# Optimization experiments

Measured on AMD Instinct MI355X. Metric: run time of the kernel, lower is better.

The kernel has to match this reference:

```python
import jax, jax.numpy as jnp
import numpy as np

B, S, D_DIM = 32, 512, 1024

def setup_inputs() -> dict:
    key = jax.random.key(0)
    k1, k2, k3, k4 = jax.random.split(key, 4)
    return {
        "D": jax.random.normal(k1, (B, S, D_DIM), dtype=jnp.float32),
        "H": jax.random.normal(k2, (B, S, D_DIM), dtype=jnp.float32),
        # learned params: U is (d+1, d) (xavier-style scale), W is (2d+1,)
        # (original inits W to zeros; we use small random values so the linear
        #  term is exercised — same math either way)
        "U": jax.random.normal(k3, (D_DIM + 1, D_DIM), dtype=jnp.float32) * 0.02,
        "W": jax.random.normal(k4, (2 * D_DIM + 1,), dtype=jnp.float32) * 0.02,
    }

def reference(D, H, U, W):
    # D, H: [B, S, d]; U: [d+1, d]; W: [2d+1]
    d = H.shape[-1]
    ones = jnp.ones(D.shape[:2] + (1,), dtype=D.dtype)
    Daug = jnp.concatenate([D, ones], axis=-1)              # [B, S, d+1]
    # bilinear term: v.U.u  -> [B, Sx, Sy]
    bil = jnp.einsum('bxi,ij,byj->bxy', Daug, U, H)
    # linear term W . concat(D_aug, H): algebraically split — avoids the
    # O(B*S*S*2d) concatenated intermediate of the original implementation
    lin = (Daug @ W[:d + 1])[:, :, None] + (H @ W[d + 1:])[:, None, :]
    return bil + lin
```

## Files before the change

kernel.cpp:

```cpp
#include <hip/hip_runtime.h>


#define D_DIM 1024
#define ROWS 16384

typedef float floatx4 __attribute__((ext_vector_type(4)));
typedef __bf16 bf16x8 __attribute__((ext_vector_type(8)));

__device__ inline unsigned short f2bf(float f) {
  unsigned int u = __builtin_bit_cast(unsigned int, f);
  u = (u + 0x7FFFu + ((u >> 16) & 1u)) >> 16;
  return (unsigned short)u;
}

__device__ inline void async_load16(const void* g, void* l) {
  __builtin_amdgcn_global_load_lds(
      (const __attribute__((address_space(1))) void*)g,
      (__attribute__((address_space(3))) void*)l, 16, 0, 0);
}

__global__ __launch_bounds__(256) void cast_rows_kernel(
    const float* __restrict__ D, const float* __restrict__ H,
    const float* __restrict__ W,
    unsigned short* __restrict__ Dbf, unsigned short* __restrict__ Hbf,
    float* __restrict__ linD, float* __restrict__ linH) {
  int rowid = blockIdx.x;
  bool isH = rowid >= ROWS;
  int r = isH ? rowid - ROWS : rowid;
  const float* src = (isH ? H : D) + (size_t)r * D_DIM;
  unsigned short* dst = (isH ? Hbf : Dbf) + (size_t)r * D_DIM;
  const float* w = W + (isH ? (D_DIM + 1) : 0);
  int t = threadIdx.x;
  float4 v = ((const float4*)src)[t];
  float s = v.x * w[4*t] + v.y * w[4*t+1] + v.z * w[4*t+2] + v.w * w[4*t+3];
  ushort4 o;
  o.x = f2bf(v.x); o.y = f2bf(v.y); o.z = f2bf(v.z); o.w = f2bf(v.w);
  ((ushort4*)dst)[t] = o;
  #pragma unroll
  for (int off = 32; off > 0; off >>= 1) s += __shfl_down(s, off, 64);
  __shared__ float red[4];
  int wave = t >> 6;
  if ((t & 63) == 0) red[wave] = s;
  __syncthreads();
  if (t == 0) {
    float tot = red[0] + red[1] + red[2] + red[3];
    if (!isH) tot += W[D_DIM];
    (isH ? linH : linD)[r] = tot;
  }
}

__global__ __launch_bounds__(256) void transU_kernel(
    const float* __restrict__ U, unsigned short* __restrict__ Ut) {
  __shared__ float tile[32][33];
  int n0 = blockIdx.x * 32;
  int k0 = blockIdx.y * 32;
  int t = threadIdx.x;
  int tr = t >> 5, tc = t & 31;
  #pragma unroll
  for (int i = 0; i < 32; i += 8)
    tile[tr + i][tc] = U[(size_t)(k0 + tr + i) * D_DIM + n0 + tc];
  __syncthreads();
  #pragma unroll
  for (int i = 0; i < 32; i += 8)
    Ut[(size_t)(n0 + tr + i) * D_DIM + k0 + tc] = f2bf(tile[tc][tr + i]);
}

template <int MWAVES, int NWAVES, int MT, int NT, int BROWS>
__device__ inline void gemm_core_swz(
    const unsigned short* __restrict__ A, const unsigned short* __restrict__ Bt,
    int m0, int n0, unsigned short* As, unsigned short* Bs,
    floatx4 (&acc)[MT][NT]) {
  const int K = D_DIM;
  int tid = threadIdx.x;
  int l = tid & 63, wave = tid >> 6;
  int quad = l >> 4, lrow = l & 15;
  int wm = (NWAVES == 2) ? (wave >> 1) : wave;
  int wn = (NWAVES == 2) ? (wave & 1) : 0;

  int srow = 8 * wave + (l >> 3);
  int sq = (l & 7) ^ (l >> 3);
  const unsigned short* gA = A + (size_t)(m0 + srow) * K + sq * 8;
  const unsigned short* gB = Bt + (size_t)(n0 + srow) * K + sq * 8;

  int rl = lrow & 7, gofs = lrow >> 3;
  int baseA = wm * (MT * 128) + gofs * 64 + rl * 8;
  int baseB = wn * (NT * 128) + gofs * 64 + rl * 8;

  for (int k0 = 0; k0 < K; k0 += 64) {
    __syncthreads();
    #pragma unroll
    for (int j = 0; j < 4; ++j)
      async_load16(gA + (size_t)(32 * j) * K + k0, As + (j * 256 + tid) * 8);
    #pragma unroll
    for (int j = 0; j < BROWS / 32; ++j)
      async_load16(gB + (size_t)(32 * j) * K + k0, Bs + (j * 256 + tid) * 8);
    __syncthreads();
    #pragma unroll
    for (int s = 0; s < 2; ++s) {
      int xq = (s * 4 + quad) ^ rl;
      bf16x8 a[MT], b[NT];
      #pragma unroll
      for (int mt = 0; mt < MT; ++mt)
        a[mt] = *(const bf16x8*)(As + (baseA + mt * 128 + xq) * 8);
      #pragma unroll
      for (int nt = 0; nt < NT; ++nt)
        b[nt] = *(const bf16x8*)(Bs + (baseB + nt * 128 + xq) * 8);
      #pragma unroll
      for (int mt = 0; mt < MT; ++mt)
        #pragma unroll
        for (int nt = 0; nt < NT; ++nt)
          acc[mt][nt] = __builtin_amdgcn_mfma_f32_16x16x32_bf16(
              a[mt], b[nt], acc[mt][nt], 0, 0, 0);
    }
  }
}

__global__ __launch_bounds__(256) void gemm1_kernel(
    const unsigned short* __restrict__ A,
    const unsigned short* __restrict__ Bt,
    const float* __restrict__ Ubias,
    unsigned short* __restrict__ T) {
  __shared__ __align__(16) unsigned short As[128 * 64];
  __shared__ __align__(16) unsigned short Bs[128 * 64];
  int m0 = blockIdx.x * 128, n0 = blockIdx.y * 128;
  int tid = threadIdx.x;
  int lane = tid & 63, wave = tid >> 6;
  int quad = lane >> 4, lrow = lane & 15;
  int wm = wave >> 1, wn = wave & 1;

  floatx4 acc[4][4] = {};
  gemm_core_swz<2, 2, 4, 4, 128>(A, Bt, m0, n0, As, Bs, acc);

  #pragma unroll
  for (int mt = 0; mt < 4; ++mt)
    #pragma unroll
    for (int nt = 0; nt < 4; ++nt) {
      int row = m0 + wm * 64 + mt * 16 + quad * 4;
      int col = n0 + wn * 64 + nt * 16 + lrow;
      float bias = Ubias[col];
      #pragma unroll
      for (int rr = 0; rr < 4; ++rr)
        T[(size_t)(row + rr) * D_DIM + col] = f2bf(acc[mt][nt][rr] + bias);
    }
}

__global__ __launch_bounds__(256) void gemm2_kernel(
    const unsigned short* __restrict__ Tg,
    const unsigned short* __restrict__ Hbf,
    const float* __restrict__ linD, const float* __restrict__ linH,
    float* __restrict__ out) {
  __shared__ __align__(16) unsigned short As[128 * 64];
  __shared__ __align__(16) unsigned short Bs[64 * 64];
  int b = blockIdx.x;
  int t = blockIdx.y;
  int m0 = (t >> 3) * 128, n0 = (t & 7) * 64;
  const unsigned short* A = Tg + (size_t)b * 512 * D_DIM;
  const unsigned short* Bt = Hbf + (size_t)b * 512 * D_DIM;
  int tid = threadIdx.x;
  int lane = tid & 63, wave = tid >> 6;
  int quad = lane >> 4, lrow = lane & 15;
  int wm = wave;

  floatx4 acc[2][4] = {};
  gemm_core_swz<4, 1, 2, 4, 64>(A, Bt, m0, n0, As, Bs, acc);

  #pragma unroll
  for (int mt = 0; mt < 2; ++mt)
    #pragma unroll
    for (int nt = 0; nt < 4; ++nt) {
      int row = m0 + wm * 32 + mt * 16 + quad * 4;
      int col = n0 + nt * 16 + lrow;
      float lh = linH[b * 512 + col];
      #pragma unroll
      for (int rr = 0; rr < 4; ++rr) {
        float v = acc[mt][nt][rr] + linD[b * 512 + row + rr] + lh;
        out[((size_t)b * 512 + row + rr) * 512 + col] = v;
      }
    }
}

extern "C" void kernel_launch(void* const* d_in, const int* in_sizes, int n_in,
                              void* d_out, int out_size, void* d_ws, size_t ws_size,
                              hipStream_t stream) {
  const float* D = (const float*)d_in[0];
  const float* H = (const float*)d_in[1];
  const float* U = (const float*)d_in[2];
  const float* W = (const float*)d_in[3];
  float* out = (float*)d_out;

  char* ws = (char*)d_ws;
  unsigned short* Dbf = (unsigned short*)ws; ws += (size_t)ROWS * D_DIM * 2;
  unsigned short* Hbf = (unsigned short*)ws; ws += (size_t)ROWS * D_DIM * 2;
  unsigned short* Tbf = (unsigned short*)ws; ws += (size_t)ROWS * D_DIM * 2;
  unsigned short* Ut  = (unsigned short*)ws; ws += (size_t)D_DIM * D_DIM * 2;
  float* linD = (float*)ws;                  ws += (size_t)ROWS * 4;
  float* linH = (float*)ws;                  ws += (size_t)ROWS * 4;

  cast_rows_kernel<<<dim3(2 * ROWS), 256, 0, stream>>>(D, H, W, Dbf, Hbf, linD, linH);
  transU_kernel<<<dim3(32, 32), 256, 0, stream>>>(U, Ut);
  gemm1_kernel<<<dim3(128, 8), 256, 0, stream>>>(Dbf, Ut, U + (size_t)D_DIM * D_DIM, Tbf);
  gemm2_kernel<<<dim3(32, 32), 256, 0, stream>>>(Tbf, Hbf, linD, linH, out);
}
```

Before: 234.1 us.

## Merge cast and U-transpose kernels, enlarge gemm2 tile, use nontemporal output stores

Folds the U transpose/cast into the row-cast kernel as extra blocks, which saves one launch. The batched second GEMM moves from 128x64 to 128x128 tiles with a 2x2 wave layout, which raises arithmetic intensity and cuts redundant A-tile loads. The grid halves to 512 blocks on the GPU's 256 CUs. Output stores become nontemporal so the large fp32 result does not pollute cache. The bigger accumulators raise register pressure, and the smaller grid may hurt occupancy.

```diff
diff --git a/kernel.cpp b/kernel.cpp
--- a/kernel.cpp
+++ b/kernel.cpp
@@ -19,50 +19,51 @@
       (__attribute__((address_space(3))) void*)l, 16, 0, 0);
 }
 
-__global__ __launch_bounds__(256) void cast_rows_kernel(
+__global__ __launch_bounds__(256) void cast_transU_kernel(
     const float* __restrict__ D, const float* __restrict__ H,
-    const float* __restrict__ W,
+    const float* __restrict__ U, const float* __restrict__ W,
     unsigned short* __restrict__ Dbf, unsigned short* __restrict__ Hbf,
+    unsigned short* __restrict__ Ut,
     float* __restrict__ linD, float* __restrict__ linH) {
-  int rowid = blockIdx.x;
-  bool isH = rowid >= ROWS;
-  int r = isH ? rowid - ROWS : rowid;
-  const float* src = (isH ? H : D) + (size_t)r * D_DIM;
-  unsigned short* dst = (isH ? Hbf : Dbf) + (size_t)r * D_DIM;
-  const float* w = W + (isH ? (D_DIM + 1) : 0);
+  __shared__ float tile[32][33];
+  int bid = blockIdx.x;
   int t = threadIdx.x;
-  float4 v = ((const float4*)src)[t];
-  float s = v.x * w[4*t] + v.y * w[4*t+1] + v.z * w[4*t+2] + v.w * w[4*t+3];
-  ushort4 o;
-  o.x = f2bf(v.x); o.y = f2bf(v.y); o.z = f2bf(v.z); o.w = f2bf(v.w);
-  ((ushort4*)dst)[t] = o;
-  #pragma unroll
-  for (int off = 32; off > 0; off >>= 1) s += __shfl_down(s, off, 64);
-  __shared__ float red[4];
-  int wave = t >> 6;
-  if ((t & 63) == 0) red[wave] = s;
-  __syncthreads();
-  if (t == 0) {
-    float tot = red[0] + red[1] + red[2] + red[3];
-    if (!isH) tot += W[D_DIM];
-    (isH ? linH : linD)[r] = tot;
+
+  if (bid < 2 * ROWS) {
+    bool isH = bid >= ROWS;
+    int r = isH ? bid - ROWS : bid;
+    const float* src = (isH ? H : D) + (size_t)r * D_DIM;
+    unsigned short* dst = (isH ? Hbf : Dbf) + (size_t)r * D_DIM;
+    const float* w = W + (isH ? (D_DIM + 1) : 0);
+    float4 v = ((const float4*)src)[t];
+    float s = v.x * w[4*t] + v.y * w[4*t+1] + v.z * w[4*t+2] + v.w * w[4*t+3];
+    ushort4 o;
+    o.x = f2bf(v.x); o.y = f2bf(v.y); o.z = f2bf(v.z); o.w = f2bf(v.w);
+    ((ushort4*)dst)[t] = o;
+    #pragma unroll
+    for (int off = 32; off > 0; off >>= 1) s += __shfl_down(s, off, 64);
+    float* red = &tile[0][0];
+    int wave = t >> 6;
+    if ((t & 63) == 0) red[wave] = s;
+    __syncthreads();
+    if (t == 0) {
+      float tot = red[0] + red[1] + red[2] + red[3];
+      if (!isH) tot += W[D_DIM];
+      (isH ? linH : linD)[r] = tot;
+    }
+  } else {
+    int tb = bid - 2 * ROWS;
+    int n0 = (tb & 31) * 32;
+    int k0 = (tb >> 5) * 32;
+    int tr = t >> 5, tc = t & 31;
+    #pragma unroll
+    for (int i = 0; i < 32; i += 8)
+      tile[tr + i][tc] = U[(size_t)(k0 + tr + i) * D_DIM + n0 + tc];
+    __syncthreads();
+    #pragma unroll
+    for (int i = 0; i < 32; i += 8)
+      Ut[(size_t)(n0 + tr + i) * D_DIM + k0 + tc] = f2bf(tile[tc][tr + i]);
   }
-}
-
-__global__ __launch_bounds__(256) void transU_kernel(
-    const float* __restrict__ U, unsigned short* __restrict__ Ut) {
-  __shared__ float tile[32][33];
-  int n0 = blockIdx.x * 32;
-  int k0 = blockIdx.y * 32;
-  int t = threadIdx.x;
-  int tr = t >> 5, tc = t & 31;
-  #pragma unroll
-  for (int i = 0; i < 32; i += 8)
-    tile[tr + i][tc] = U[(size_t)(k0 + tr + i) * D_DIM + n0 + tc];
-  __syncthreads();
-  #pragma unroll
-  for (int i = 0; i < 32; i += 8)
-    Ut[(size_t)(n0 + tr + i) * D_DIM + k0 + tc] = f2bf(tile[tc][tr + i]);
 }
 
 template <int MWAVES, int NWAVES, int MT, int NT, int BROWS>
@@ -150,31 +151,32 @@
     const float* __restrict__ linD, const float* __restrict__ linH,
     float* __restrict__ out) {
   __shared__ __align__(16) unsigned short As[128 * 64];
-  __shared__ __align__(16) unsigned short Bs[64 * 64];
+  __shared__ __align__(16) unsigned short Bs[128 * 64];
   int b = blockIdx.x;
   int t = blockIdx.y;
-  int m0 = (t >> 3) * 128, n0 = (t & 7) * 64;
+  int m0 = (t >> 2) * 128, n0 = (t & 3) * 128;
   const unsigned short* A = Tg + (size_t)b * 512 * D_DIM;
   const unsigned short* Bt = Hbf + (size_t)b * 512 * D_DIM;
   int tid = threadIdx.x;
   int lane = tid & 63, wave = tid >> 6;
   int quad = lane >> 4, lrow = lane & 15;
-  int wm = wave;
-
-  floatx4 acc[2][4] = {};
-  gemm_core_swz<4, 1, 2, 4, 64>(A, Bt, m0, n0, As, Bs, acc);
+  int wm = wave >> 1, wn = wave & 1;
+
+  floatx4 acc[4][4] = {};
+  gemm_core_swz<2, 2, 4, 4, 128>(A, Bt, m0, n0, As, Bs, acc);
 
   #pragma unroll
-  for (int mt = 0; mt < 2; ++mt)
+  for (int mt = 0; mt < 4; ++mt)
     #pragma unroll
     for (int nt = 0; nt < 4; ++nt) {
-      int row = m0 + wm * 32 + mt * 16 + quad * 4;
-      int col = n0 + nt * 16 + lrow;
+      int row = m0 + wm * 64 + mt * 16 + quad * 4;
+      int col = n0 + wn * 64 + nt * 16 + lrow;
       float lh = linH[b * 512 + col];
       #pragma unroll
       for (int rr = 0; rr < 4; ++rr) {
         float v = acc[mt][nt][rr] + linD[b * 512 + row + rr] + lh;
-        out[((size_t)b * 512 + row + rr) * 512 + col] = v;
+        __builtin_nontemporal_store(
+            v, &out[((size_t)b * 512 + row + rr) * 512 + col]);
       }
     }
 }
@@ -196,8 +198,8 @@
   float* linD = (float*)ws;                  ws += (size_t)ROWS * 4;
   float* linH = (float*)ws;                  ws += (size_t)ROWS * 4;
 
-  cast_rows_kernel<<<dim3(2 * ROWS), 256, 0, stream>>>(D, H, W, Dbf, Hbf, linD, linH);
-  transU_kernel<<<dim3(32, 32), 256, 0, stream>>>(U, Ut);
+  cast_transU_kernel<<<dim3(2 * ROWS + 1024), 256, 0, stream>>>(
+      D, H, U, W, Dbf, Hbf, Ut, linD, linH);
   gemm1_kernel<<<dim3(128, 8), 256, 0, stream>>>(Dbf, Ut, U + (size_t)D_DIM * D_DIM, Tbf);
-  gemm2_kernel<<<dim3(32, 32), 256, 0, stream>>>(Tbf, Hbf, linD, linH, out);
-}
+  gemm2_kernel<<<dim3(32, 16), 256, 0, stream>>>(Tbf, Hbf, linD, linH, out);
+}
```

After: 224.3 us. 1.04x faster.
